# Performance work log

Hardware: AMD Instinct MI355X
Metric: run time of the kernel (lower is better)

Reference implementation:

```python
import jax, jax.numpy as jnp
import numpy as np
from jax.scipy.special import logsumexp

NUM_STATES = 16
NUM_CHAINS = 8
NUM_NODES = 1500
NUM_ITERS = 500


def setup_inputs() -> dict:
    key = jax.random.key(0)
    k1, k2, k3, k4 = jax.random.split(key, 4)
    return {
        "unnormalized_state_init": jax.random.normal(k1, (NUM_STATES, NUM_CHAINS), jnp.float32),
        "unnormalized_chain_weights": jax.random.normal(k2, (NUM_ITERS, NUM_CHAINS), jnp.float32),
        "unnormalized_emission_matrix": jax.random.normal(k3, (NUM_STATES, 1, NUM_NODES), jnp.float32),
        "unnormalized_transition_matrix": jax.random.normal(k4, (NUM_CHAINS, NUM_STATES, NUM_STATES), jnp.float32),
    }


def reference(unnormalized_state_init, unnormalized_chain_weights,
              unnormalized_emission_matrix, unnormalized_transition_matrix):
    # log_transform_params: normalize each distribution in log domain
    log_state_init = jax.nn.log_softmax(unnormalized_state_init, axis=0)          # (S,C): over states
    log_chain_weights = jax.nn.log_softmax(unnormalized_chain_weights, axis=-1)   # (T,C): over chains
    log_emission = jax.nn.log_softmax(unnormalized_emission_matrix, axis=-1)      # (S,1,N): over nodes
    log_T_ = jax.nn.log_softmax(unnormalized_transition_matrix, axis=-1)          # (C,S,S): over next state

    T = unnormalized_chain_weights.shape[0]

    # chain-marginalized transition matrix (computed as in torch forward_model; not used downstream)
    log_mean_cw = logsumexp(log_chain_weights, axis=0) - jnp.log(jnp.asarray(T, log_chain_weights.dtype))
    _log_transition_matrix = logsumexp(log_T_ + log_mean_cw[:, None, None], axis=0)

    # sequential HMM prior recursion over tiny (S,C) state via scan
    def step(h, _):
        # h: (S,C) -> h.T: (C,S); logsumexp over previous-state axis
        new = logsumexp(h.T[:, :, None] + log_T_, axis=1).T  # (S,C)
        return new, new

    h0 = log_state_init
    _, hs = jax.lax.scan(step, h0, None, length=T - 1)
    log_hidden_state_probs = jnp.concatenate([h0[None], hs], axis=0)  # (T,S,C)

    # emission broadcast: (S,1,N) + (T,S,C,1) -> (T,S,C,N), then add chain weights
    log_observed_state_probs_ = (log_emission[None]
                                 + log_hidden_state_probs[..., None]
                                 + log_chain_weights[:, None, :, None])
    # marginalize over states then chains
    log_observed_state_probs = logsumexp(log_observed_state_probs_, axis=(1, 2))  # (T,N)
    return (log_observed_state_probs, log_observed_state_probs_, log_hidden_state_probs)
```

## Files before the change

### kernel.cpp

```cpp
#include <hip/hip_runtime.h>
#include <hip/hip_bf16.h>

#define S 16
#define C 8
#define SC 128
#define TT 500
#define NN 1500
#define NF4 375
#define CHUNK 25
#define NCHUNK 20

__device__ __forceinline__ float fexp2(float x) { return exp2f(x); }
__device__ __forceinline__ float flog2(float x) { return log2f(x); }

#define L2E 1.4426950408889634f
#define LN2 0.6931471805599453f

typedef float f4v __attribute__((ext_vector_type(4)));

#define MM(dst, Asrc, Bsrc) do {                                          \
    __syncthreads();                                                      \
    {   const int c_ = tid >> 5; const int e0_ = tid & 31;                \
        for (int r_ = 0; r_ < 8; ++r_) {                                  \
            const int e_ = e0_ + (r_ << 5);                               \
            const int i_ = e_ >> 4; const int l_ = e_ & 15;               \
            float acc_ = 0.f;                                             \
            _Pragma("unroll")                                             \
            for (int s_ = 0; s_ < S; ++s_)                                \
                acc_ += Asrc[(c_ * S + i_) * S + s_] *                    \
                        Bsrc[(c_ * S + s_) * S + l_];                     \
            dst[(c_ * S + i_) * S + l_] = acc_;                          \
        } }                                                               \
} while (0)

__global__ __launch_bounds__(256) void hmm_setup(
    const float* __restrict__ usi,
    const float* __restrict__ ucw,
    const float* __restrict__ uem,
    const float* __restrict__ utm,
    float* __restrict__ ws_lcw,
    float* __restrict__ ws_pT,
    float* __restrict__ ws_q,
    float* __restrict__ ws_emlse)
{
    __shared__ float bufT[C * S * S];
    __shared__ float bufX[C * S * S];
    __shared__ float bufY[C * S * S];
    __shared__ float bufZ[C * S * S];
    __shared__ float qbuf[C * S];
    const int tid = threadIdx.x;

    for (int t = tid; t < TT; t += 256) {
        float x[C]; float m = -1e30f;
#pragma unroll
        for (int cc = 0; cc < C; ++cc) { x[cc] = ucw[t * C + cc]; m = fmaxf(m, x[cc]); }
        float acc = 0.f;
#pragma unroll
        for (int cc = 0; cc < C; ++cc) acc += fexp2((x[cc] - m) * L2E);
        const float lse = m + flog2(acc) * LN2;
#pragma unroll
        for (int cc = 0; cc < C; ++cc) ws_lcw[t * C + cc] = x[cc] - lse;
    }

    {
        const int row = tid >> 4;
        const int ln  = tid & 15;
        const float* rp = uem + row * NN;
        float a = 0.f;
        for (int n = ln; n < NN; n += 16) a += fexp2(rp[n] * L2E);
#pragma unroll
        for (int off = 8; off >= 1; off >>= 1) a += __shfl_xor(a, off);
        if (ln == 0) ws_emlse[row] = flog2(a) * LN2;
    }

    if (tid < SC) {
        float x[S]; float m = -1e30f;
#pragma unroll
        for (int k = 0; k < S; ++k) { x[k] = utm[tid * S + k]; m = fmaxf(m, x[k]); }
        float acc = 0.f; float e[S];
#pragma unroll
        for (int k = 0; k < S; ++k) { e[k] = fexp2((x[k] - m) * L2E); acc += e[k]; }
        const float inv = 1.f / acc;
#pragma unroll
        for (int k = 0; k < S; ++k) {
            const float v = e[k] * inv;
            bufT[tid * S + k] = v;
            ws_pT[tid * S + k] = v;
        }
    }

    if (tid < C) {
        const int cc = tid;
        float x[S]; float m = -1e30f;
#pragma unroll
        for (int s0 = 0; s0 < S; ++s0) { x[s0] = usi[s0 * C + cc]; m = fmaxf(m, x[s0]); }
        float acc = 0.f; float e[S];
#pragma unroll
        for (int s0 = 0; s0 < S; ++s0) { e[s0] = fexp2((x[s0] - m) * L2E); acc += e[s0]; }
        const float inv = 1.f / acc;
#pragma unroll
        for (int s0 = 0; s0 < S; ++s0) {
            const float v = e[s0] * inv;
            qbuf[cc * S + s0] = v;
            ws_q[cc * S + s0] = v;
        }
    }

    MM(bufX, bufT, bufT);
    MM(bufY, bufX, bufX);
    MM(bufZ, bufY, bufY);
    MM(bufX, bufZ, bufZ);
    MM(bufY, bufX, bufZ);
    MM(bufX, bufY, bufT);
    __syncthreads();

    const int c5 = tid >> 4;
    const int l5 = tid & 15;
    float Acol[S];
    if (tid < 128) {
#pragma unroll
        for (int s0 = 0; s0 < S; ++s0) Acol[s0] = bufX[(c5 * S + s0) * S + l5];
    }
    for (int k = 1; k < NCHUNK; ++k) {
        float acc = 0.f;
        if (tid < 128) {
#pragma unroll
            for (int s0 = 0; s0 < S; ++s0) acc += qbuf[c5 * S + s0] * Acol[s0];
        }
        __syncthreads();
        if (tid < 128) {
            qbuf[c5 * S + l5] = acc;
            ws_q[k * SC + c5 * S + l5] = acc;
        }
        __syncthreads();
    }
}

__global__ __launch_bounds__(64) void hmm_chunks(
    const float* __restrict__ ws_pT,
    const float* __restrict__ ws_q,
    float* __restrict__ out3)
{
    const int k = blockIdx.x;
    const int lane = threadIdx.x;
    const int c = lane >> 3;
    const int j = lane & 7;

    float Ta[S], Tb[S];
#pragma unroll
    for (int s0 = 0; s0 < S; ++s0) {
        Ta[s0] = ws_pT[(c * S + s0) * S + j];
        Tb[s0] = ws_pT[(c * S + s0) * S + j + 8];
    }
    float pa = ws_q[k * SC + c * S + j];
    float pb = ws_q[k * SC + c * S + j + 8];

    const int base = c << 3;
    for (int i = 0; i < CHUNK; ++i) {
        float* o = out3 + (size_t)(k * CHUNK + i) * SC;
        o[j * C + c]       = flog2(pa) * LN2;
        o[(j + 8) * C + c] = flog2(pb) * LN2;
        if (i == CHUNK - 1) break;

        float pv[S];
#pragma unroll
        for (int q = 0; q < 8; ++q) {
            pv[q]     = __shfl(pa, base + q);
            pv[q + 8] = __shfl(pb, base + q);
        }
        float a0 = 0.f, a1 = 0.f, a2 = 0.f, a3 = 0.f;
        float b0 = 0.f, b1 = 0.f, b2 = 0.f, b3 = 0.f;
#pragma unroll
        for (int s0 = 0; s0 < S; s0 += 4) {
            a0 = fmaf(pv[s0],     Ta[s0],     a0);
            a1 = fmaf(pv[s0 + 1], Ta[s0 + 1], a1);
            a2 = fmaf(pv[s0 + 2], Ta[s0 + 2], a2);
            a3 = fmaf(pv[s0 + 3], Ta[s0 + 3], a3);
            b0 = fmaf(pv[s0],     Tb[s0],     b0);
            b1 = fmaf(pv[s0 + 1], Tb[s0 + 1], b1);
            b2 = fmaf(pv[s0 + 2], Tb[s0 + 2], b2);
            b3 = fmaf(pv[s0 + 3], Tb[s0 + 3], b3);
        }
        pa = (a0 + a1) + (a2 + a3);
        pb = (b0 + b1) + (b2 + b3);
    }
}

__global__ __launch_bounds__(128) void broadcast_kernel(
    const float* __restrict__ uem,
    const float* __restrict__ lcw,
    const float* __restrict__ h3,
    const float* __restrict__ ws_emlse,
    float* __restrict__ out1,
    float* __restrict__ out2)
{
    const int t = blockIdx.y;
    const int tid = threadIdx.x;
    __shared__ float hc[SC];
    __shared__ float Ws[S];
    __shared__ float emS[S];
    if (tid < SC) hc[tid] = h3[t * SC + tid] + lcw[t * C + (tid & 7)];
    if (tid < S) emS[tid] = ws_emlse[tid];
    __syncthreads();
    if (tid < S) {
        float m = -1e30f;
#pragma unroll
        for (int cc = 0; cc < C; ++cc) m = fmaxf(m, hc[tid * C + cc]);
        float acc = 0.f;
#pragma unroll
        for (int cc = 0; cc < C; ++cc) acc += fexp2((hc[tid * C + cc] - m) * L2E);
        Ws[tid] = m + flog2(acc) * LN2;
    }
    __syncthreads();

    const int n4 = blockIdx.x * 128 + tid;
    if (n4 >= NF4) return;

    float4 es[S];
#pragma unroll
    for (int s0 = 0; s0 < S; ++s0) {
        float4 e = ((const float4*)(uem + s0 * NN))[n4];
        const float el = emS[s0];
        e.x -= el; e.y -= el; e.z -= el; e.w -= el;
        es[s0] = e;
    }

    float* o2 = out2 + (size_t)t * SC * NN + 4 * n4;
#pragma unroll
    for (int s0 = 0; s0 < S; ++s0) {
#pragma unroll
        for (int cc = 0; cc < C; ++cc) {
            const float hv = hc[s0 * C + cc];
            f4v v;
            v.x = es[s0].x + hv; v.y = es[s0].y + hv;
            v.z = es[s0].z + hv; v.w = es[s0].w + hv;
            __builtin_nontemporal_store(v, (f4v*)(o2 + (size_t)(s0 * C + cc) * NN));
        }
    }

    float4 mv = make_float4(-1e30f, -1e30f, -1e30f, -1e30f);
    float4 xs[S];
#pragma unroll
    for (int s0 = 0; s0 < S; ++s0) {
        const float w = Ws[s0];
        xs[s0].x = es[s0].x + w; mv.x = fmaxf(mv.x, xs[s0].x);
        xs[s0].y = es[s0].y + w; mv.y = fmaxf(mv.y, xs[s0].y);
        xs[s0].z = es[s0].z + w; mv.z = fmaxf(mv.z, xs[s0].z);
        xs[s0].w = es[s0].w + w; mv.w = fmaxf(mv.w, xs[s0].w);
    }
    float4 av = make_float4(0.f, 0.f, 0.f, 0.f);
#pragma unroll
    for (int s0 = 0; s0 < S; ++s0) {
        av.x += fexp2((xs[s0].x - mv.x) * L2E);
        av.y += fexp2((xs[s0].y - mv.y) * L2E);
        av.z += fexp2((xs[s0].z - mv.z) * L2E);
        av.w += fexp2((xs[s0].w - mv.w) * L2E);
    }
    float4 r;
    r.x = mv.x + flog2(av.x) * LN2;
    r.y = mv.y + flog2(av.y) * LN2;
    r.z = mv.z + flog2(av.z) * LN2;
    r.w = mv.w + flog2(av.w) * LN2;
    *(float4*)(out1 + (size_t)t * NN + 4 * n4) = r;
}

extern "C" void kernel_launch(void* const* d_in, const int* in_sizes, int n_in,
                              void* d_out, int out_size, void* d_ws, size_t ws_size,
                              hipStream_t stream)
{
    const float* usi = (const float*)d_in[0];
    const float* ucw = (const float*)d_in[1];
    const float* uem = (const float*)d_in[2];
    const float* utm = (const float*)d_in[3];

    float* out  = (float*)d_out;
    float* out1 = out;
    float* out2 = out + 750000;
    float* out3 = out + 750000 + 96000000;

    float* ws       = (float*)d_ws;
    float* ws_lcw   = ws;
    float* ws_pT    = ws + 4000;
    float* ws_q     = ws + 6048;
    float* ws_emlse = ws + 8608;

    hmm_setup<<<1, 256, 0, stream>>>(usi, ucw, uem, utm,
                                     ws_lcw, ws_pT, ws_q, ws_emlse);
    hmm_chunks<<<NCHUNK, 64, 0, stream>>>(ws_pT, ws_q, out3);
    broadcast_kernel<<<dim3(3, TT), 128, 0, stream>>>(uem, ws_lcw, out3, ws_emlse,
                                                      out1, out2);
}
```

Measured before the change: 148.8 us.

## Fuse setup, chunk recursion and broadcast into one kernel per timestep

Replaces the three-kernel pipeline with a single kernel of one 384-thread block per timestep. Each block recomputes the normalized transition matrix, its 25th power, and the initial state, jumps to its chunk with repeated matrix-vector products, then steps forward up to 24 times to get its own hidden state. This removes two launches and the serial single-block setup, in exchange for redundant per-block recomputation and longer serial chains in late blocks. It also switches the large output writes from nontemporal to ordinary stores.

```diff
diff --git a/kernel.cpp b/kernel.cpp
--- a/kernel.cpp
+++ b/kernel.cpp
@@ -8,7 +8,6 @@
 #define NN 1500
 #define NF4 375
 #define CHUNK 25
-#define NCHUNK 20
 
 __device__ __forceinline__ float fexp2(float x) { return exp2f(x); }
 __device__ __forceinline__ float flog2(float x) { return log2f(x); }
@@ -20,90 +19,83 @@
 
 #define MM(dst, Asrc, Bsrc) do {                                          \
     __syncthreads();                                                      \
-    {   const int c_ = tid >> 5; const int e0_ = tid & 31;                \
-        for (int r_ = 0; r_ < 8; ++r_) {                                  \
-            const int e_ = e0_ + (r_ << 5);                               \
-            const int i_ = e_ >> 4; const int l_ = e_ & 15;               \
-            float acc_ = 0.f;                                             \
-            _Pragma("unroll")                                             \
-            for (int s_ = 0; s_ < S; ++s_)                                \
-                acc_ += Asrc[(c_ * S + i_) * S + s_] *                    \
-                        Bsrc[(c_ * S + s_) * S + l_];                     \
-            dst[(c_ * S + i_) * S + l_] = acc_;                          \
-        } }                                                               \
+    for (int e_ = tid; e_ < 2048; e_ += 384) {                            \
+        const int c_ = e_ >> 8;                                           \
+        const int i_ = (e_ >> 4) & 15;                                    \
+        const int l_ = e_ & 15;                                           \
+        float acc_ = 0.f;                                                 \
+        _Pragma("unroll")                                                 \
+        for (int s_ = 0; s_ < S; ++s_)                                    \
+            acc_ += Asrc[(c_ * S + i_) * S + s_] *                        \
+                    Bsrc[(c_ * S + s_) * S + l_];                         \
+        dst[(c_ * S + i_) * S + l_] = acc_;                              \
+    }                                                                     \
 } while (0)
 
-__global__ __launch_bounds__(256) void hmm_setup(
+__global__ __launch_bounds__(384) void fused_all(
     const float* __restrict__ usi,
     const float* __restrict__ ucw,
     const float* __restrict__ uem,
     const float* __restrict__ utm,
-    float* __restrict__ ws_lcw,
-    float* __restrict__ ws_pT,
-    float* __restrict__ ws_q,
-    float* __restrict__ ws_emlse)
+    float* __restrict__ out1,
+    float* __restrict__ out2,
+    float* __restrict__ out3)
 {
+    const int t = blockIdx.x;
+    const int tid = threadIdx.x;
     __shared__ float bufT[C * S * S];
     __shared__ float bufX[C * S * S];
     __shared__ float bufY[C * S * S];
     __shared__ float bufZ[C * S * S];
-    __shared__ float qbuf[C * S];
-    const int tid = threadIdx.x;
-
-    for (int t = tid; t < TT; t += 256) {
+    __shared__ float qbuf[SC];
+    __shared__ float hc[SC];
+    __shared__ float Ws[S];
+    __shared__ float emS[S];
+    __shared__ float lcwS[C];
+
+    if (tid < SC) {
+        float x[S]; float m = -1e30f;
+#pragma unroll
+        for (int k = 0; k < S; ++k) { x[k] = utm[tid * S + k]; m = fmaxf(m, x[k]); }
+        float acc = 0.f; float e[S];
+#pragma unroll
+        for (int k = 0; k < S; ++k) { e[k] = fexp2((x[k] - m) * L2E); acc += e[k]; }
+        const float inv = 1.f / acc;
+#pragma unroll
+        for (int k = 0; k < S; ++k) bufT[tid * S + k] = e[k] * inv;
+    }
+    if (tid < C) {
+        const int cc = tid;
+        float x[S]; float m = -1e30f;
+#pragma unroll
+        for (int s0 = 0; s0 < S; ++s0) { x[s0] = usi[s0 * C + cc]; m = fmaxf(m, x[s0]); }
+        float acc = 0.f; float e[S];
+#pragma unroll
+        for (int s0 = 0; s0 < S; ++s0) { e[s0] = fexp2((x[s0] - m) * L2E); acc += e[s0]; }
+        const float inv = 1.f / acc;
+#pragma unroll
+        for (int s0 = 0; s0 < S; ++s0) qbuf[cc * S + s0] = e[s0] * inv;
+    }
+    if (tid >= 8 && tid < 16) {
+        const int cc = tid - 8;
         float x[C]; float m = -1e30f;
 #pragma unroll
-        for (int cc = 0; cc < C; ++cc) { x[cc] = ucw[t * C + cc]; m = fmaxf(m, x[cc]); }
+        for (int k = 0; k < C; ++k) { x[k] = ucw[t * C + k]; m = fmaxf(m, x[k]); }
         float acc = 0.f;
 #pragma unroll
-        for (int cc = 0; cc < C; ++cc) acc += fexp2((x[cc] - m) * L2E);
-        const float lse = m + flog2(acc) * LN2;
-#pragma unroll
-        for (int cc = 0; cc < C; ++cc) ws_lcw[t * C + cc] = x[cc] - lse;
-    }
-
-    {
-        const int row = tid >> 4;
-        const int ln  = tid & 15;
+        for (int k = 0; k < C; ++k) acc += fexp2((x[k] - m) * L2E);
+        lcwS[cc] = x[cc] - (m + flog2(acc) * LN2);
+    }
+    if (tid >= SC) {
+        const int u   = tid - SC;
+        const int row = u >> 4;
+        const int ln  = u & 15;
         const float* rp = uem + row * NN;
         float a = 0.f;
         for (int n = ln; n < NN; n += 16) a += fexp2(rp[n] * L2E);
 #pragma unroll
         for (int off = 8; off >= 1; off >>= 1) a += __shfl_xor(a, off);
-        if (ln == 0) ws_emlse[row] = flog2(a) * LN2;
-    }
-
-    if (tid < SC) {
-        float x[S]; float m = -1e30f;
-#pragma unroll
-        for (int k = 0; k < S; ++k) { x[k] = utm[tid * S + k]; m = fmaxf(m, x[k]); }
-        float acc = 0.f; float e[S];
-#pragma unroll
-        for (int k = 0; k < S; ++k) { e[k] = fexp2((x[k] - m) * L2E); acc += e[k]; }
-        const float inv = 1.f / acc;
-#pragma unroll
-        for (int k = 0; k < S; ++k) {
-            const float v = e[k] * inv;
-            bufT[tid * S + k] = v;
-            ws_pT[tid * S + k] = v;
-        }
-    }
-
-    if (tid < C) {
-        const int cc = tid;
-        float x[S]; float m = -1e30f;
-#pragma unroll
-        for (int s0 = 0; s0 < S; ++s0) { x[s0] = usi[s0 * C + cc]; m = fmaxf(m, x[s0]); }
-        float acc = 0.f; float e[S];
-#pragma unroll
-        for (int s0 = 0; s0 < S; ++s0) { e[s0] = fexp2((x[s0] - m) * L2E); acc += e[s0]; }
-        const float inv = 1.f / acc;
-#pragma unroll
-        for (int s0 = 0; s0 < S; ++s0) {
-            const float v = e[s0] * inv;
-            qbuf[cc * S + s0] = v;
-            ws_q[cc * S + s0] = v;
-        }
+        if (ln == 0) emS[row] = flog2(a) * LN2;
     }
 
     MM(bufX, bufT, bufT);
@@ -114,94 +106,70 @@
     MM(bufX, bufY, bufT);
     __syncthreads();
 
+    const int kq = t / CHUNK;
     const int c5 = tid >> 4;
     const int l5 = tid & 15;
     float Acol[S];
-    if (tid < 128) {
+    if (tid < SC) {
 #pragma unroll
         for (int s0 = 0; s0 < S; ++s0) Acol[s0] = bufX[(c5 * S + s0) * S + l5];
     }
-    for (int k = 1; k < NCHUNK; ++k) {
+    for (int k = 0; k < kq; ++k) {
         float acc = 0.f;
-        if (tid < 128) {
+        if (tid < SC) {
 #pragma unroll
             for (int s0 = 0; s0 < S; ++s0) acc += qbuf[c5 * S + s0] * Acol[s0];
         }
         __syncthreads();
-        if (tid < 128) {
-            qbuf[c5 * S + l5] = acc;
-            ws_q[k * SC + c5 * S + l5] = acc;
-        }
+        if (tid < SC) qbuf[c5 * S + l5] = acc;
         __syncthreads();
     }
-}
-
-__global__ __launch_bounds__(64) void hmm_chunks(
-    const float* __restrict__ ws_pT,
-    const float* __restrict__ ws_q,
-    float* __restrict__ out3)
-{
-    const int k = blockIdx.x;
-    const int lane = threadIdx.x;
-    const int c = lane >> 3;
-    const int j = lane & 7;
-
-    float Ta[S], Tb[S];
-#pragma unroll
-    for (int s0 = 0; s0 < S; ++s0) {
-        Ta[s0] = ws_pT[(c * S + s0) * S + j];
-        Tb[s0] = ws_pT[(c * S + s0) * S + j + 8];
-    }
-    float pa = ws_q[k * SC + c * S + j];
-    float pb = ws_q[k * SC + c * S + j + 8];
-
-    const int base = c << 3;
-    for (int i = 0; i < CHUNK; ++i) {
-        float* o = out3 + (size_t)(k * CHUNK + i) * SC;
-        o[j * C + c]       = flog2(pa) * LN2;
-        o[(j + 8) * C + c] = flog2(pb) * LN2;
-        if (i == CHUNK - 1) break;
-
-        float pv[S];
-#pragma unroll
-        for (int q = 0; q < 8; ++q) {
-            pv[q]     = __shfl(pa, base + q);
-            pv[q + 8] = __shfl(pb, base + q);
-        }
-        float a0 = 0.f, a1 = 0.f, a2 = 0.f, a3 = 0.f;
-        float b0 = 0.f, b1 = 0.f, b2 = 0.f, b3 = 0.f;
-#pragma unroll
-        for (int s0 = 0; s0 < S; s0 += 4) {
-            a0 = fmaf(pv[s0],     Ta[s0],     a0);
-            a1 = fmaf(pv[s0 + 1], Ta[s0 + 1], a1);
-            a2 = fmaf(pv[s0 + 2], Ta[s0 + 2], a2);
-            a3 = fmaf(pv[s0 + 3], Ta[s0 + 3], a3);
-            b0 = fmaf(pv[s0],     Tb[s0],     b0);
-            b1 = fmaf(pv[s0 + 1], Tb[s0 + 1], b1);
-            b2 = fmaf(pv[s0 + 2], Tb[s0 + 2], b2);
-            b3 = fmaf(pv[s0 + 3], Tb[s0 + 3], b3);
-        }
-        pa = (a0 + a1) + (a2 + a3);
-        pb = (b0 + b1) + (b2 + b3);
-    }
-}
-
-__global__ __launch_bounds__(128) void broadcast_kernel(
-    const float* __restrict__ uem,
-    const float* __restrict__ lcw,
-    const float* __restrict__ h3,
-    const float* __restrict__ ws_emlse,
-    float* __restrict__ out1,
-    float* __restrict__ out2)
-{
-    const int t = blockIdx.y;
-    const int tid = threadIdx.x;
-    __shared__ float hc[SC];
-    __shared__ float Ws[S];
-    __shared__ float emS[S];
-    if (tid < SC) hc[tid] = h3[t * SC + tid] + lcw[t * C + (tid & 7)];
-    if (tid < S) emS[tid] = ws_emlse[tid];
+
+    if (tid < 64) {
+        const int c = tid >> 3;
+        const int j = tid & 7;
+        float Ta[S], Tb[S];
+#pragma unroll
+        for (int s0 = 0; s0 < S; ++s0) {
+            Ta[s0] = bufT[(c * S + s0) * S + j];
+            Tb[s0] = bufT[(c * S + s0) * S + j + 8];
+        }
+        float pa = qbuf[c * S + j];
+        float pb = qbuf[c * S + j + 8];
+        const int base = c << 3;
+        const int m = t - kq * CHUNK;
+        for (int i = 0; i < m; ++i) {
+            float pv[S];
+#pragma unroll
+            for (int q = 0; q < 8; ++q) {
+                pv[q]     = __shfl(pa, base + q);
+                pv[q + 8] = __shfl(pb, base + q);
+            }
+            float a0 = 0.f, a1 = 0.f, a2 = 0.f, a3 = 0.f;
+            float b0 = 0.f, b1 = 0.f, b2 = 0.f, b3 = 0.f;
+#pragma unroll
+            for (int s0 = 0; s0 < S; s0 += 4) {
+                a0 = fmaf(pv[s0],     Ta[s0],     a0);
+                a1 = fmaf(pv[s0 + 1], Ta[s0 + 1], a1);
+                a2 = fmaf(pv[s0 + 2], Ta[s0 + 2], a2);
+                a3 = fmaf(pv[s0 + 3], Ta[s0 + 3], a3);
+                b0 = fmaf(pv[s0],     Tb[s0],     b0);
+                b1 = fmaf(pv[s0 + 1], Tb[s0 + 1], b1);
+                b2 = fmaf(pv[s0 + 2], Tb[s0 + 2], b2);
+                b3 = fmaf(pv[s0 + 3], Tb[s0 + 3], b3);
+            }
+            pa = (a0 + a1) + (a2 + a3);
+            pb = (b0 + b1) + (b2 + b3);
+        }
+        const float la = flog2(pa) * LN2;
+        const float lb = flog2(pb) * LN2;
+        out3[(size_t)t * SC + j * C + c]       = la;
+        out3[(size_t)t * SC + (j + 8) * C + c] = lb;
+        hc[j * C + c]       = la + lcwS[c];
+        hc[(j + 8) * C + c] = lb + lcwS[c];
+    }
     __syncthreads();
+
     if (tid < S) {
         float m = -1e30f;
 #pragma unroll
@@ -213,7 +181,7 @@
     }
     __syncthreads();
 
-    const int n4 = blockIdx.x * 128 + tid;
+    const int n4 = tid;
     if (n4 >= NF4) return;
 
     float4 es[S];
@@ -231,10 +199,10 @@
 #pragma unroll
         for (int cc = 0; cc < C; ++cc) {
             const float hv = hc[s0 * C + cc];
-            f4v v;
+            float4 v;
             v.x = es[s0].x + hv; v.y = es[s0].y + hv;
             v.z = es[s0].z + hv; v.w = es[s0].w + hv;
-            __builtin_nontemporal_store(v, (f4v*)(o2 + (size_t)(s0 * C + cc) * NN));
+            *(float4*)(o2 + (size_t)(s0 * C + cc) * NN) = v;
         }
     }
 
@@ -278,15 +246,5 @@
     float* out2 = out + 750000;
     float* out3 = out + 750000 + 96000000;
 
-    float* ws       = (float*)d_ws;
-    float* ws_lcw   = ws;
-    float* ws_pT    = ws + 4000;
-    float* ws_q     = ws + 6048;
-    float* ws_emlse = ws + 8608;
-
-    hmm_setup<<<1, 256, 0, stream>>>(usi, ucw, uem, utm,
-                                     ws_lcw, ws_pT, ws_q, ws_emlse);
-    hmm_chunks<<<NCHUNK, 64, 0, stream>>>(ws_pT, ws_q, out3);
-    broadcast_kernel<<<dim3(3, TT), 128, 0, stream>>>(uem, ws_lcw, out3, ws_emlse,
-                                                      out1, out2);
+    fused_all<<<TT, 384, 0, stream>>>(usi, ucw, uem, utm, out1, out2, out3);
 }
```

New measurement: 128.8 us. 1.16x faster.

## Replace chunked HMM recursion with binary matrix powers computed per block

Applied to the files above, without the earlier changes.

The setup kernel now computes the transition matrix raised to powers of two (T^1..T^256) by repeated squaring and stores them. Each broadcast block then derives its own hidden-state vector by multiplying the initial distribution by the powers selected from the bits of t, which removes the separate hmm_chunks kernel and its launch. It also swaps the nontemporal output stores for plain float4 stores. The trade-offs are that up to nine small matrix-vector products with barriers are repeated in every block, and that the blocks along x redundantly recompute and write the same out3 row.

```diff
diff --git a/kernel.cpp b/kernel.cpp
--- a/kernel.cpp
+++ b/kernel.cpp
@@ -7,8 +7,7 @@
 #define TT 500
 #define NN 1500
 #define NF4 375
-#define CHUNK 25
-#define NCHUNK 20
+#define NPOW 9
 
 __device__ __forceinline__ float fexp2(float x) { return exp2f(x); }
 __device__ __forceinline__ float flog2(float x) { return log2f(x); }
@@ -39,15 +38,12 @@
     const float* __restrict__ uem,
     const float* __restrict__ utm,
     float* __restrict__ ws_lcw,
-    float* __restrict__ ws_pT,
-    float* __restrict__ ws_q,
-    float* __restrict__ ws_emlse)
+    float* __restrict__ ws_emlse,
+    float* __restrict__ ws_p0,
+    float* __restrict__ ws_P)
 {
-    __shared__ float bufT[C * S * S];
-    __shared__ float bufX[C * S * S];
-    __shared__ float bufY[C * S * S];
-    __shared__ float bufZ[C * S * S];
-    __shared__ float qbuf[C * S];
+    __shared__ float bufA[C * S * S];
+    __shared__ float bufB[C * S * S];
     const int tid = threadIdx.x;
 
     for (int t = tid; t < TT; t += 256) {
@@ -84,8 +80,8 @@
 #pragma unroll
         for (int k = 0; k < S; ++k) {
             const float v = e[k] * inv;
-            bufT[tid * S + k] = v;
-            ws_pT[tid * S + k] = v;
+            bufA[tid * S + k] = v;
+            ws_P[tid * S + k] = v;
         }
     }
 
@@ -99,109 +95,65 @@
         for (int s0 = 0; s0 < S; ++s0) { e[s0] = fexp2((x[s0] - m) * L2E); acc += e[s0]; }
         const float inv = 1.f / acc;
 #pragma unroll
-        for (int s0 = 0; s0 < S; ++s0) {
-            const float v = e[s0] * inv;
-            qbuf[cc * S + s0] = v;
-            ws_q[cc * S + s0] = v;
-        }
-    }
-
-    MM(bufX, bufT, bufT);
-    MM(bufY, bufX, bufX);
-    MM(bufZ, bufY, bufY);
-    MM(bufX, bufZ, bufZ);
-    MM(bufY, bufX, bufZ);
-    MM(bufX, bufY, bufT);
-    __syncthreads();
-
-    const int c5 = tid >> 4;
-    const int l5 = tid & 15;
-    float Acol[S];
-    if (tid < 128) {
-#pragma unroll
-        for (int s0 = 0; s0 < S; ++s0) Acol[s0] = bufX[(c5 * S + s0) * S + l5];
-    }
-    for (int k = 1; k < NCHUNK; ++k) {
-        float acc = 0.f;
-        if (tid < 128) {
-#pragma unroll
-            for (int s0 = 0; s0 < S; ++s0) acc += qbuf[c5 * S + s0] * Acol[s0];
-        }
+        for (int s0 = 0; s0 < S; ++s0) ws_p0[cc * S + s0] = e[s0] * inv;
+    }
+
+    for (int k = 1; k < NPOW; ++k) {
+        if (k & 1) { MM(bufB, bufA, bufA); }
+        else       { MM(bufA, bufB, bufB); }
         __syncthreads();
-        if (tid < 128) {
-            qbuf[c5 * S + l5] = acc;
-            ws_q[k * SC + c5 * S + l5] = acc;
-        }
-        __syncthreads();
-    }
-}
-
-__global__ __launch_bounds__(64) void hmm_chunks(
-    const float* __restrict__ ws_pT,
-    const float* __restrict__ ws_q,
-    float* __restrict__ out3)
-{
-    const int k = blockIdx.x;
-    const int lane = threadIdx.x;
-    const int c = lane >> 3;
-    const int j = lane & 7;
-
-    float Ta[S], Tb[S];
-#pragma unroll
-    for (int s0 = 0; s0 < S; ++s0) {
-        Ta[s0] = ws_pT[(c * S + s0) * S + j];
-        Tb[s0] = ws_pT[(c * S + s0) * S + j + 8];
-    }
-    float pa = ws_q[k * SC + c * S + j];
-    float pb = ws_q[k * SC + c * S + j + 8];
-
-    const int base = c << 3;
-    for (int i = 0; i < CHUNK; ++i) {
-        float* o = out3 + (size_t)(k * CHUNK + i) * SC;
-        o[j * C + c]       = flog2(pa) * LN2;
-        o[(j + 8) * C + c] = flog2(pb) * LN2;
-        if (i == CHUNK - 1) break;
-
-        float pv[S];
-#pragma unroll
-        for (int q = 0; q < 8; ++q) {
-            pv[q]     = __shfl(pa, base + q);
-            pv[q + 8] = __shfl(pb, base + q);
-        }
-        float a0 = 0.f, a1 = 0.f, a2 = 0.f, a3 = 0.f;
-        float b0 = 0.f, b1 = 0.f, b2 = 0.f, b3 = 0.f;
-#pragma unroll
-        for (int s0 = 0; s0 < S; s0 += 4) {
-            a0 = fmaf(pv[s0],     Ta[s0],     a0);
-            a1 = fmaf(pv[s0 + 1], Ta[s0 + 1], a1);
-            a2 = fmaf(pv[s0 + 2], Ta[s0 + 2], a2);
-            a3 = fmaf(pv[s0 + 3], Ta[s0 + 3], a3);
-            b0 = fmaf(pv[s0],     Tb[s0],     b0);
-            b1 = fmaf(pv[s0 + 1], Tb[s0 + 1], b1);
-            b2 = fmaf(pv[s0 + 2], Tb[s0 + 2], b2);
-            b3 = fmaf(pv[s0 + 3], Tb[s0 + 3], b3);
-        }
-        pa = (a0 + a1) + (a2 + a3);
-        pb = (b0 + b1) + (b2 + b3);
+        const float* src = (k & 1) ? bufB : bufA;
+        float* dst = ws_P + k * (C * S * S);
+        for (int e = tid; e < C * S * S; e += 256) dst[e] = src[e];
     }
 }
 
 __global__ __launch_bounds__(128) void broadcast_kernel(
     const float* __restrict__ uem,
-    const float* __restrict__ lcw,
-    const float* __restrict__ h3,
+    const float* __restrict__ ws_lcw,
     const float* __restrict__ ws_emlse,
+    const float* __restrict__ ws_p0,
+    const float* __restrict__ ws_P,
     float* __restrict__ out1,
-    float* __restrict__ out2)
+    float* __restrict__ out2,
+    float* __restrict__ out3)
 {
     const int t = blockIdx.y;
     const int tid = threadIdx.x;
+    __shared__ float v0[SC];
+    __shared__ float v1[SC];
     __shared__ float hc[SC];
     __shared__ float Ws[S];
     __shared__ float emS[S];
-    if (tid < SC) hc[tid] = h3[t * SC + tid] + lcw[t * C + (tid & 7)];
+
+    v0[tid] = ws_p0[tid];
     if (tid < S) emS[tid] = ws_emlse[tid];
     __syncthreads();
+
+    float* vin = v0;
+    float* vout = v1;
+    const int c = tid >> 4;
+    const int sp = tid & 15;
+#pragma unroll
+    for (int k = 0; k < NPOW; ++k) {
+        if ((t >> k) & 1) {
+            const float* Pk = ws_P + k * (C * S * S) + c * (S * S) + sp;
+            float acc = 0.f;
+#pragma unroll
+            for (int s0 = 0; s0 < S; ++s0) acc += vin[c * S + s0] * Pk[s0 * S];
+            vout[tid] = acc;
+            float* tmp = vin; vin = vout; vout = tmp;
+            __syncthreads();
+        }
+    }
+
+    {
+        const float lv = flog2(vin[tid]) * LN2;
+        out3[(size_t)t * SC + sp * C + c] = lv;
+        hc[sp * C + c] = lv + ws_lcw[t * C + c];
+    }
+    __syncthreads();
+
     if (tid < S) {
         float m = -1e30f;
 #pragma unroll
@@ -231,10 +183,10 @@
 #pragma unroll
         for (int cc = 0; cc < C; ++cc) {
             const float hv = hc[s0 * C + cc];
-            f4v v;
+            float4 v;
             v.x = es[s0].x + hv; v.y = es[s0].y + hv;
             v.z = es[s0].z + hv; v.w = es[s0].w + hv;
-            __builtin_nontemporal_store(v, (f4v*)(o2 + (size_t)(s0 * C + cc) * NN));
+            *(float4*)(o2 + (size_t)(s0 * C + cc) * NN) = v;
         }
     }
 
@@ -280,13 +232,13 @@
 
     float* ws       = (float*)d_ws;
     float* ws_lcw   = ws;
-    float* ws_pT    = ws + 4000;
-    float* ws_q     = ws + 6048;
-    float* ws_emlse = ws + 8608;
+    float* ws_emlse = ws + 4000;
+    float* ws_p0    = ws + 4016;
+    float* ws_P     = ws + 4144;
 
     hmm_setup<<<1, 256, 0, stream>>>(usi, ucw, uem, utm,
-                                     ws_lcw, ws_pT, ws_q, ws_emlse);
-    hmm_chunks<<<NCHUNK, 64, 0, stream>>>(ws_pT, ws_q, out3);
-    broadcast_kernel<<<dim3(3, TT), 128, 0, stream>>>(uem, ws_lcw, out3, ws_emlse,
-                                                      out1, out2);
+                                     ws_lcw, ws_emlse, ws_p0, ws_P);
+    broadcast_kernel<<<dim3(3, TT), 128, 0, stream>>>(uem, ws_lcw, ws_emlse,
+                                                      ws_p0, ws_P,
+                                                      out1, out2, out3);
 }
```

After: 138.7 us. 6.8% less time.
